# Kernel tuning notes

Hardware: AMD Instinct MI355X
Metric: run time of the kernel (lower is better)

The kernel has to match this reference:

```python
import jax, jax.numpy as jnp
import numpy as np
import math

B, S, E, H = 1, 4096, 1024, 16
D = E // H  # head_dim = 64

def setup_inputs() -> dict:
    key = jax.random.key(0)
    kx, kq, kk, kv, ko = jax.random.split(key, 5)
    sc = 1.0 / math.sqrt(E)
    return {
        "x": jax.random.normal(kx, (B, S, E), dtype=jnp.float32),
        "Wq": jax.random.normal(kq, (E, E), dtype=jnp.float32) * sc,
        "Wk": jax.random.normal(kk, (E, E), dtype=jnp.float32) * sc,
        "Wv": jax.random.normal(kv, (E, E), dtype=jnp.float32) * sc,
        "Wo": jax.random.normal(ko, (E, E), dtype=jnp.float32) * sc,
    }

def reference(x, Wq, Wk, Wv, Wo):
    b, s, _ = x.shape
    # nn.Linear(no bias): x @ W.T ; then split heads -> [b, H, s, D]
    def heads(w):
        return (x @ w.T).reshape(b, s, H, D).transpose(0, 2, 1, 3)
    q, k, v = heads(Wq), heads(Wk), heads(Wv)
    scale = 1.0 / math.sqrt(D)
    logits = jnp.einsum('bhqd,bhkd->bhqk', q, k) * scale  # [b,H,s,s]
    causal = jnp.tril(jnp.ones((s, s), dtype=bool))
    logits = jnp.where(causal, logits, -jnp.inf)
    attn = jax.nn.softmax(logits, axis=-1)
    out = jnp.einsum('bhqk,bhkd->bhqd', attn, v)  # [b,H,s,D]
    out = out.transpose(0, 2, 1, 3).reshape(b, s, E)
    return out @ Wo.T
```

## Files before the change

### kernel.cpp

```cpp
#include <hip/hip_runtime.h>
#include <hip/hip_bf16.h>

typedef unsigned short u16;
typedef unsigned int u32;
typedef __attribute__((ext_vector_type(8))) short short8;
typedef __attribute__((ext_vector_type(4))) float f32x4;
typedef __attribute__((ext_vector_type(16))) float f32x16;
typedef __attribute__((ext_vector_type(4))) u32 u32x4;
typedef __attribute__((ext_vector_type(2))) u32 u32x2;


__device__ __forceinline__ u16 f2b(float f) {
  unsigned u = __float_as_uint(f);
  u = (u + 0x7FFFu + ((u >> 16) & 1u)) >> 16;
  return (u16)u;
}

__device__ __forceinline__ u32 pkbf(float lo, float hi) {
  __hip_bfloat162 b = __float22bfloat162_rn(make_float2(lo, hi));
  u32 r;
  __builtin_memcpy(&r, &b, 4);
  return r;
}

__device__ __forceinline__ u32x2 plswap(u32 a, u32 b) {
  return __builtin_amdgcn_permlane32_swap(a, b, false, false);
}

__device__ __forceinline__ void gload16(const void* g, void* l) {
  __builtin_amdgcn_global_load_lds(
      (const __attribute__((address_space(1))) void*)g,
      (__attribute__((address_space(3))) void*)l, 16, 0, 0);
}


__global__ __launch_bounds__(256) void cvt_all_kernel(
    const float* __restrict__ x, const float* __restrict__ w0,
    const float* __restrict__ w1, const float* __restrict__ w2,
    const float* __restrict__ w3, u16* __restrict__ xo, u16* __restrict__ o0,
    u16* __restrict__ o1, u16* __restrict__ o2, u16* __restrict__ o3,
    float scale0) {
  const int bid = blockIdx.x;
  const float* in;
  u16* out;
  float scale = 1.f;
  int i;
  if (bid < 4096) {
    in = x; out = xo; i = bid;
  } else {
    const int k = (bid - 4096) >> 10;
    i = (bid - 4096) & 1023;
    in = (k == 0) ? w0 : (k == 1) ? w1 : (k == 2) ? w2 : w3;
    out = (k == 0) ? o0 : (k == 1) ? o1 : (k == 2) ? o2 : o3;
    if (k == 0) scale = scale0;
  }
  int idx = (i * 256 + threadIdx.x) * 4;
  float4 v = *(const float4*)(in + idx);
  unsigned p0 = (unsigned)f2b(v.x * scale) | ((unsigned)f2b(v.y * scale) << 16);
  unsigned p1 = (unsigned)f2b(v.z * scale) | ((unsigned)f2b(v.w * scale) << 16);
  *(uint2*)(out + idx) = make_uint2(p0, p1);
}


__global__ __launch_bounds__(256) void transpose_kernel(const u16* __restrict__ V,
                                                        u16* __restrict__ Vt) {
  __shared__ u16 t[32][33];
  int bx = blockIdx.x;
  int by = blockIdx.y;
  int c = threadIdx.x & 31, r4 = threadIdx.x >> 5;
#pragma unroll
  for (int i = 0; i < 4; ++i) {
    int row = r4 * 4 + i;
    t[row][c] = V[(size_t)(by * 32 + row) * 1024 + bx * 32 + c];
  }
  __syncthreads();
#pragma unroll
  for (int i = 0; i < 4; ++i) {
    int row = r4 * 4 + i;
    Vt[(size_t)(bx * 32 + row) * 4096 + by * 32 + c] = t[c][row];
  }
}


__device__ __forceinline__ void storeC(u16* C, size_t idx, float v) { C[idx] = f2b(v); }
__device__ __forceinline__ void storeC(float* C, size_t idx, float v) { C[idx] = v; }

template <int BN, typename OutT>
__device__ __forceinline__ void gemm_body(const u16* __restrict__ A,
                                          const u16* __restrict__ B,
                                          OutT* __restrict__ C) {
  constexpr int NF = BN / 32;
  constexpr int BJ = BN / 32;
  __shared__ __align__(16) u16 lA[128 * 64];
  __shared__ __align__(16) u16 lB[BN * 64];
  const int tid = threadIdx.x;
  const int w = tid >> 6, lane = tid & 63, g = lane >> 4, lr = lane & 15;
  const int wr = w >> 1, wc = w & 1;
  const int m0 = blockIdx.y * 128, n0 = blockIdx.x * BN;

  f32x4 acc[4][NF] = {};

  for (int k0 = 0; k0 < 1024; k0 += 64) {
#pragma unroll
    for (int j = 0; j < 4; ++j) {
      int c = tid + j * 256;
      int row = c >> 3, sub = (c & 7) ^ (row & 7);
      gload16(A + (size_t)(m0 + row) * 1024 + k0 + sub * 8,
              &lA[(j * 256 + w * 64) * 8]);
      if (j < BJ)
        gload16(B + (size_t)(n0 + row) * 1024 + k0 + sub * 8,
                &lB[(j * 256 + w * 64) * 8]);
    }
    __syncthreads();

#pragma unroll
    for (int k2 = 0; k2 < 2; ++k2) {
      short8 af[4], bf[NF];
#pragma unroll
      for (int i = 0; i < 4; ++i) {
        int row = wr * 64 + i * 16 + lr;
        af[i] = *(const short8*)&lA[row * 64 + ((((k2 << 2) | g) ^ (row & 7)) << 3)];
      }
#pragma unroll
      for (int i = 0; i < NF; ++i) {
        int row = wc * (BN / 2) + i * 16 + lr;
        bf[i] = *(const short8*)&lB[row * 64 + ((((k2 << 2) | g) ^ (row & 7)) << 3)];
      }
#pragma unroll
      for (int mi = 0; mi < 4; ++mi)
#pragma unroll
        for (int ni = 0; ni < NF; ++ni)
          acc[mi][ni] = __builtin_amdgcn_mfma_f32_16x16x32_bf16(af[mi], bf[ni],
                                                                acc[mi][ni], 0, 0, 0);
    }
    __syncthreads();
  }

#pragma unroll
  for (int mi = 0; mi < 4; ++mi)
#pragma unroll
    for (int ni = 0; ni < NF; ++ni)
#pragma unroll
      for (int r = 0; r < 4; ++r) {
        size_t row = (size_t)(m0 + wr * 64 + mi * 16 + g * 4 + r);
        size_t col = (size_t)(n0 + wc * (BN / 2) + ni * 16 + lr);
        storeC(C, row * 1024 + col, acc[mi][ni][r]);
      }
}

__global__ __launch_bounds__(256) void gemm_qkv_kernel(
    const u16* __restrict__ A, const u16* __restrict__ W0, const u16* __restrict__ W1,
    const u16* __restrict__ W2, u16* __restrict__ C0, u16* __restrict__ C1,
    u16* __restrict__ C2) {
  int z = blockIdx.z;
  const u16* B = (z == 0) ? W0 : (z == 1) ? W1 : W2;
  u16* C = (z == 0) ? C0 : (z == 1) ? C1 : C2;
  gemm_body<128, u16>(A, B, C);
}

__global__ __launch_bounds__(256) void gemm_out_kernel(const u16* __restrict__ A,
                                                       const u16* __restrict__ B,
                                                       float* __restrict__ C) {
  gemm_body<64, float>(A, B, C);
}


#define NEGINF (-30000.0f)

__global__ __launch_bounds__(512, 4) void attn_kernel(const u16* __restrict__ Qg,
                                                      const u16* __restrict__ Kg,
                                                      const u16* __restrict__ Vtg,
                                                      u16* __restrict__ Og) {
  __shared__ __align__(16) char smem[65536];

  const int tid = threadIdx.x, lane = tid & 63;
  const int w8 = tid >> 6, p = w8 >> 2, qw = w8 & 3;
  const int l31 = lane & 31, hi = lane >> 5;
  const int bid = blockIdx.x;
  const int h = bid & 15;
  const int i32 = bid >> 4;
  const int qb = (i32 < 16) ? (31 - i32) : (i32 - 16);
  const int qs = qb * 128;
  const int qsw = qs + qw * 32;
  const int iters = qb + 1;
  const int kstart = p ? iters : 0;
  const int dtw = qsw >> 6;
  const int swz = (l31 & 7) << 4;

  const u32x4 onesu = {0x3F803F80u, 0x3F803F80u, 0x3F803F80u, 0x3F803F80u};
  const short8 ones = __builtin_bit_cast(short8, onesu);

  short8 qf[4];
  {
    const u16* Qp = Qg + (size_t)(qsw + l31) * 1024 + h * 64 + hi * 8;
#pragma unroll
    for (int kc = 0; kc < 4; ++kc) qf[kc] = *(const short8*)(Qp + kc * 16);
  }

  const int j0 = qw * 2;
  auto stage = [&](int b, int kt) {
    char* Kb = smem + (((p << 1) | b) << 14);
    char* Vb = Kb + 8192;
#pragma unroll
    for (int jj = 0; jj < 2; ++jj) {
      const int j = j0 + jj;
      const int row = (j << 3) + (lane >> 3);
      const int c = (lane & 7) ^ (row & 7);
      gload16(Kg + (size_t)(kt * 64 + row) * 1024 + h * 64 + c * 8,
              Kb + (j << 10));
      gload16(Vtg + (size_t)(h * 64 + row) * 4096 + kt * 64 + c * 8,
              Vb + (j << 10));
    }
  };

  f32x16 ot[2] = {};
  f32x16 lacc = {};

  int cur = 0;
  stage(0, kstart);
  __syncthreads();

  for (int it = 0; it < iters; ++it) {
    const int kt = kstart + it;
    if (it + 1 < iters) stage(cur ^ 1, kt + 1);

    const bool doCompute = (p == 0) || (kt <= dtw);
    if (doCompute) {
      const char* Kb = smem + (((p << 1) | cur) << 14);
      const char* Vb = Kb + 8192;

      f32x16 st0 = {}, st1 = {};
#pragma unroll
      for (int kc = 0; kc < 4; ++kc) {
        short8 k0 = *(const short8*)(Kb + l31 * 128 + ((((kc << 1) | hi) << 4) ^ swz));
        st0 = __builtin_amdgcn_mfma_f32_32x32x16_bf16(k0, qf[kc], st0, 0, 0, 0);
      }
#pragma unroll
      for (int kc = 0; kc < 4; ++kc) {
        short8 k1 =
            *(const short8*)(Kb + 4096 + l31 * 128 + ((((kc << 1) | hi) << 4) ^ swz));
        st1 = __builtin_amdgcn_mfma_f32_32x32x16_bf16(k1, qf[kc], st1, 0, 0, 0);
      }

      if (kt == dtw) {
        const int q = qsw + l31;
#pragma unroll
        for (int r = 0; r < 16; ++r) {
          int key = kt * 64 + (r & 3) + 8 * (r >> 2) + 4 * hi;
          if (key > q) st0[r] = NEGINF;
          if (key + 32 > q) st1[r] = NEGINF;
        }
      }

#pragma unroll
      for (int r = 0; r < 16; ++r) {
        st0[r] = __builtin_amdgcn_exp2f(st0[r] - 12.f);
        st1[r] = __builtin_amdgcn_exp2f(st1[r] - 12.f);
      }

#pragma unroll
      for (int kt2 = 0; kt2 < 2; ++kt2) {
        const f32x16& st = kt2 ? st1 : st0;
        short8 pa[2];
#pragma unroll
        for (int ks = 0; ks < 2; ++ks) {
          const int b = 8 * ks;
          u32 pk0 = pkbf(st[b + 0], st[b + 1]);
          u32 pk1 = pkbf(st[b + 2], st[b + 3]);
          u32 pk2 = pkbf(st[b + 4], st[b + 5]);
          u32 pk3 = pkbf(st[b + 6], st[b + 7]);
          u32x2 r02 = plswap(pk0, pk2);
          u32x2 r13 = plswap(pk1, pk3);
          u32x4 t;
          t.x = r02.x;
          t.y = r13.x;
          t.z = r02.y;
          t.w = r13.y;
          pa[ks] = __builtin_bit_cast(short8, t);
        }
        lacc = __builtin_amdgcn_mfma_f32_32x32x16_bf16(ones, pa[0], lacc, 0, 0, 0);
        lacc = __builtin_amdgcn_mfma_f32_32x32x16_bf16(ones, pa[1], lacc, 0, 0, 0);
#pragma unroll
        for (int dt = 0; dt < 2; ++dt)
#pragma unroll
          for (int ks = 0; ks < 2; ++ks) {
            short8 vfv = *(const short8*)(Vb + dt * 4096 + l31 * 128 +
                                          (((kt2 * 4 + ks * 2 + hi) << 4) ^ swz));
            ot[dt] =
                __builtin_amdgcn_mfma_f32_32x32x16_bf16(vfv, pa[ks], ot[dt], 0, 0, 0);
          }
      }
    }
    __syncthreads();
    cur ^= 1;
  }

  __syncthreads();
  float* lOfw = (float*)smem + (qw << 11);
  char* pw = smem + 32768 + (qw << 12);
  float* lll = (float*)(smem + 49152) + (qw << 5);
  if (p == 0) {
#pragma unroll
    for (int dt = 0; dt < 2; ++dt)
#pragma unroll
      for (int r = 0; r < 16; ++r) {
        int d = dt * 32 + (r & 3) + 8 * (r >> 2) + 4 * hi;
        lOfw[d * 32 + l31] = ot[dt][r];
      }
    if (hi == 0) lll[l31] = lacc[0];
  }
  __syncthreads();
  if (p == 1) {
    float inv = 1.0f / (lll[l31] + lacc[0]);
#pragma unroll
    for (int dt = 0; dt < 2; ++dt)
#pragma unroll
      for (int r = 0; r < 16; ++r) {
        int d = dt * 32 + (r & 3) + 8 * (r >> 2) + 4 * hi;
        float val = (lOfw[d * 32 + l31] + ot[dt][r]) * inv;
        *(u16*)(pw + l31 * 128 + ((d * 2) ^ ((l31 & 7) << 4))) = f2b(val);
      }
  }
  __syncthreads();
  if (p == 1) {
    const int row = lane >> 1;
#pragma unroll
    for (int ii = 0; ii < 4; ++ii) {
      int c = (lane & 1) * 4 + ii;
      short8 v = *(const short8*)(pw + row * 128 + ((c * 16) ^ ((row & 7) << 4)));
      *(short8*)(Og + (size_t)(qsw + row) * 1024 + h * 64 + c * 8) = v;
    }
  }
}


extern "C" void kernel_launch(void* const* d_in, const int* in_sizes, int n_in,
                              void* d_out, int out_size, void* d_ws, size_t ws_size,
                              hipStream_t stream) {
  const float* x = (const float*)d_in[0];
  const float* Wq = (const float*)d_in[1];
  const float* Wk = (const float*)d_in[2];
  const float* Wv = (const float*)d_in[3];
  const float* Wo = (const float*)d_in[4];
  float* out = (float*)d_out;
  char* ws = (char*)d_ws;
  const size_t MB = 1024 * 1024;

  u16* xb  = (u16*)(ws);
  u16* wqb = (u16*)(ws + 8 * MB);
  u16* wkb = (u16*)(ws + 10 * MB);
  u16* wvb = (u16*)(ws + 12 * MB);
  u16* wob = (u16*)(ws + 14 * MB);
  u16* Qb  = (u16*)(ws + 16 * MB);
  u16* Kb  = (u16*)(ws + 24 * MB);
  u16* Vb  = (u16*)(ws + 32 * MB);
  u16* Vtb = (u16*)(ws + 40 * MB);
  u16* att = xb;

  const float qscale = 0.125f * 1.4426950408889634f;

  cvt_all_kernel<<<8192, 256, 0, stream>>>(x, Wq, Wk, Wv, Wo, xb, wqb, wkb, wvb,
                                           wob, qscale);

  gemm_qkv_kernel<<<dim3(8, 32, 3), 256, 0, stream>>>(xb, wqb, wkb, wvb, Qb, Kb,
                                                      Vb);
  transpose_kernel<<<dim3(32, 128), 256, 0, stream>>>(Vb, Vtb);
  attn_kernel<<<512, 512, 0, stream>>>(Qb, Kb, Vtb, att);
  gemm_out_kernel<<<dim3(16, 32), 256, 0, stream>>>(att, wob, out);
}
```

Baseline: 131.4 us.

## Stage K/V through registers into a single LDS buffer to raise occupancy

Replaces the double-buffered async global-to-LDS K/V staging with register prefetch of the next tile, written into a single LDS buffer after a barrier. The partial output exchanged between the two key-half wave groups is stored as bf16 instead of fp32. Together these roughly halve shared memory per block so more blocks can be resident per CU. The cost is an extra barrier per iteration, more live registers for the prefetch, and some precision loss in the partial-sum exchange.

```diff
diff --git a/kernel.cpp b/kernel.cpp
--- a/kernel.cpp
+++ b/kernel.cpp
@@ -14,6 +14,10 @@
   unsigned u = __float_as_uint(f);
   u = (u + 0x7FFFu + ((u >> 16) & 1u)) >> 16;
   return (u16)u;
+}
+
+__device__ __forceinline__ float b2f(u16 b) {
+  return __uint_as_float(((u32)b) << 16);
 }
 
 __device__ __forceinline__ u32 pkbf(float lo, float hi) {
@@ -171,7 +175,7 @@
                                                       const u16* __restrict__ Kg,
                                                       const u16* __restrict__ Vtg,
                                                       u16* __restrict__ Og) {
-  __shared__ __align__(16) char smem[65536];
+  __shared__ __align__(16) char smem[33280];
 
   const int tid = threadIdx.x, lane = tid & 63;
   const int w8 = tid >> 6, p = w8 >> 2, qw = w8 & 3;
@@ -198,37 +202,42 @@
   }
 
   const int j0 = qw * 2;
-  auto stage = [&](int b, int kt) {
-    char* Kb = smem + (((p << 1) | b) << 14);
-    char* Vb = Kb + 8192;
+  u32x4 kreg[2], vreg[2];
+  char* Kb = smem + (p << 14);
+  char* Vb = Kb + 8192;
+
+  auto load_regs = [&](int kt) {
 #pragma unroll
     for (int jj = 0; jj < 2; ++jj) {
       const int j = j0 + jj;
       const int row = (j << 3) + (lane >> 3);
       const int c = (lane & 7) ^ (row & 7);
-      gload16(Kg + (size_t)(kt * 64 + row) * 1024 + h * 64 + c * 8,
-              Kb + (j << 10));
-      gload16(Vtg + (size_t)(h * 64 + row) * 4096 + kt * 64 + c * 8,
-              Vb + (j << 10));
+      kreg[jj] = *(const u32x4*)(Kg + (size_t)(kt * 64 + row) * 1024 + h * 64 + c * 8);
+      vreg[jj] = *(const u32x4*)(Vtg + (size_t)(h * 64 + row) * 4096 + kt * 64 + c * 8);
+    }
+  };
+  auto write_regs = [&]() {
+#pragma unroll
+    for (int jj = 0; jj < 2; ++jj) {
+      const int j = j0 + jj;
+      *(u32x4*)(Kb + (j << 10) + (lane << 4)) = kreg[jj];
+      *(u32x4*)(Vb + (j << 10) + (lane << 4)) = vreg[jj];
     }
   };
 
   f32x16 ot[2] = {};
   f32x16 lacc = {};
 
-  int cur = 0;
-  stage(0, kstart);
+  load_regs(kstart);
+  write_regs();
   __syncthreads();
 
   for (int it = 0; it < iters; ++it) {
     const int kt = kstart + it;
-    if (it + 1 < iters) stage(cur ^ 1, kt + 1);
+    if (it + 1 < iters) load_regs(kt + 1);
 
     const bool doCompute = (p == 0) || (kt <= dtw);
     if (doCompute) {
-      const char* Kb = smem + (((p << 1) | cur) << 14);
-      const char* Vb = Kb + 8192;
-
       f32x16 st0 = {}, st1 = {};
 #pragma unroll
       for (int kc = 0; kc < 4; ++kc) {
@@ -292,20 +301,20 @@
       }
     }
     __syncthreads();
-    cur ^= 1;
-  }
-
-  __syncthreads();
-  float* lOfw = (float*)smem + (qw << 11);
-  char* pw = smem + 32768 + (qw << 12);
-  float* lll = (float*)(smem + 49152) + (qw << 5);
+    if (it + 1 < iters) write_regs();
+    __syncthreads();
+  }
+
+  u16* lOfw = (u16*)(smem) + (qw << 11);
+  char* pw = smem + 16384 + (qw << 12);
+  float* lll = (float*)(smem + 32768) + (qw << 5);
   if (p == 0) {
 #pragma unroll
     for (int dt = 0; dt < 2; ++dt)
 #pragma unroll
       for (int r = 0; r < 16; ++r) {
         int d = dt * 32 + (r & 3) + 8 * (r >> 2) + 4 * hi;
-        lOfw[d * 32 + l31] = ot[dt][r];
+        lOfw[d * 32 + l31] = f2b(ot[dt][r]);
       }
     if (hi == 0) lll[l31] = lacc[0];
   }
@@ -317,7 +326,7 @@
 #pragma unroll
       for (int r = 0; r < 16; ++r) {
         int d = dt * 32 + (r & 3) + 8 * (r >> 2) + 4 * hi;
-        float val = (lOfw[d * 32 + l31] + ot[dt][r]) * inv;
+        float val = (b2f(lOfw[d * 32 + l31]) + ot[dt][r]) * inv;
         *(u16*)(pw + l31 * 128 + ((d * 2) ^ ((l31 & 7) << 4))) = f2b(val);
       }
   }
```

New measurement: 161.5 us. 1.23x slower.
